# Optimization experiments

Measured on AMD Instinct MI355X. Metric: run time of the kernel, lower is better.

The kernel has to match this reference:

```python
import jax, jax.numpy as jnp
import numpy as np

SEQ_LEN = 12
E, H, BOTTLE = 64, 128, 1024
G, P = 64, 24
B = G * P
EPS = 1e-12  # F.normalize eps


def setup_inputs() -> dict:
    key = jax.random.key(0)
    ks = jax.random.split(key, 24)
    r = lambda k, s: (jax.random.normal(k, s, dtype=jnp.float32) * 0.1)
    starts = np.arange(G, dtype=np.int64) * P
    seq_start_end = jnp.asarray(np.stack([starts, starts + P], axis=1))
    return {
        'last_pos': jax.random.normal(ks[0], (B, 2), dtype=jnp.float32),
        'last_pos_rel': jax.random.normal(ks[1], (B, 2), dtype=jnp.float32),
        'h0': jax.random.normal(ks[2], (1, B, H), dtype=jnp.float32),
        'c0': jax.random.normal(ks[3], (1, B, H), dtype=jnp.float32),
        'seq_start_end': seq_start_end,
        # decoder spatial embedding Linear(2, E)
        'W_emb': r(ks[4], (E, 2)), 'b_emb': r(ks[5], (E,)),
        # LSTM(E -> H), gates ordered i,f,g,o as in torch
        'W_ih': r(ks[6], (4 * H, E)), 'W_hh': r(ks[7], (4 * H, H)),
        'b_ih': r(ks[8], (4 * H,)), 'b_hh': r(ks[9], (4 * H,)),
        # hidden2pos Linear(H, 2)
        'W_pos': r(ks[10], (2, H)), 'b_pos': r(ks[11], (2,)),
        # pool_net spatial embedding Linear(2, E)
        'Wp_emb': r(ks[12], (E, 2)), 'bp_emb': r(ks[13], (E,)),
        # pool_net mlp_pre_pool: (E+H)->512->1024, ReLU
        'Wp1': r(ks[14], (512, E + H)), 'bp1': r(ks[15], (512,)),
        'Wp2': r(ks[16], (BOTTLE, 512)), 'bp2': r(ks[17], (BOTTLE,)),
        # decoder mlp: (H+BOTTLE)->1024->H, ReLU
        'Wm1': r(ks[18], (1024, H + BOTTLE)), 'bm1': r(ks[19], (1024,)),
        'Wm2': r(ks[20], (H, 1024)), 'bm2': r(ks[21], (H,)),
    }


def reference(last_pos, last_pos_rel, h0, c0, seq_start_end,
              W_emb, b_emb, W_ih, W_hh, b_ih, b_hh, W_pos, b_pos,
              Wp_emb, bp_emb, Wp1, bp1, Wp2, bp2, Wm1, bm1, Wm2, bm2):
    batch = last_pos.shape[0]
    n_grp = seq_start_end.shape[0]
    n_ped = batch // n_grp  # equal contiguous groups -> static reshape
    h_dim = h0.shape[-1]

    def pool_net(h, pos):
        # h: [B,H], pos: [B,2]; groups are contiguous slices of size n_ped
        pos_g = pos.reshape(n_grp, n_ped, 2)
        hid_g = h.reshape(n_grp, n_ped, h_dim)
        # rel[g,i,j] = pos[g,j] - pos[g,i]  (torch repeat semantics)
        rel = pos_g[:, None, :, :] - pos_g[:, :, None, :]  # [G,P,P,2]
        nrm = jnp.linalg.norm(rel, axis=-1, keepdims=True)
        rel = rel / jnp.maximum(nrm, EPS)
        emb = rel @ Wp_emb.T + bp_emb                       # [G,P,P,E]
        hid_b = jnp.broadcast_to(hid_g[:, None, :, :], (n_grp, n_ped, n_ped, h_dim))
        x = jnp.concatenate([emb, hid_b], axis=-1)          # [G,P,P,E+H]
        x = jax.nn.relu(x @ Wp1.T + bp1)
        x = jax.nn.relu(x @ Wp2.T + bp2)                    # [G,P,P,1024]
        return jnp.max(x, axis=2).reshape(batch, -1)        # max over j

    def lstm_step(x, h, c):
        gates = x @ W_ih.T + b_ih + h @ W_hh.T + b_hh
        i, f, g, o = jnp.split(gates, 4, axis=-1)
        c = jax.nn.sigmoid(f) * c + jax.nn.sigmoid(i) * jnp.tanh(g)
        h = jax.nn.sigmoid(o) * jnp.tanh(c)
        return h, c

    def step(carry, _):
        h, c, lp, dec_in = carry
        h, c = lstm_step(dec_in, h, c)
        rel_pos = h @ W_pos.T + b_pos          # [B,2]
        curr_pos = rel_pos + lp
        pool_h = pool_net(h, curr_pos)         # [B,1024]
        dh = jnp.concatenate([h, pool_h], axis=1)
        dh = jax.nn.relu(dh @ Wm1.T + bm1)
        h = jax.nn.relu(dh @ Wm2.T + bm2)      # refreshed hidden state
        dec_in = rel_pos @ W_emb.T + b_emb
        return (h, c, curr_pos, dec_in), rel_pos

    dec_in0 = last_pos_rel @ W_emb.T + b_emb
    (h, c, lp, di), rels = jax.lax.scan(
        step, (h0[0], c0[0], last_pos, dec_in0), None, length=SEQ_LEN)
    return rels, h[None]  # ([seq_len,B,2], [1,B,H])
```

## Files before the change

### kernel.cpp

```cpp
#include <hip/hip_runtime.h>
#include <hip/hip_bf16.h>

typedef __attribute__((ext_vector_type(4))) float f32x4;
typedef __attribute__((ext_vector_type(8))) _Float16 f16x8;

static __device__ __forceinline__ unsigned short h2u(_Float16 h) {
  union { _Float16 h; unsigned short u; } v; v.h = h; return v.u;
}

#define MFMA16(a, b, c) __builtin_amdgcn_mfma_f32_16x16x32_f16(a, b, c, 0, 0, 0)


__global__ void build_wg(const float* __restrict__ W_ih, const float* __restrict__ W_hh,
                         _Float16* __restrict__ Wg) {
  int i = blockIdx.x * 256 + threadIdx.x;
  if (i < 512 * 192) {
    int r = i / 192, k = i % 192;
    float v = (k < 64) ? W_ih[r * 64 + k] : W_hh[r * 128 + (k - 64)];
    _Float16 h = (_Float16)v;
    Wg[i] = h;
    Wg[512 * 192 + i] = (_Float16)(v - (float)h);
  }
}

__global__ void build_wp1b(const float* __restrict__ Wp1, _Float16* __restrict__ W) {
  int i = blockIdx.x * 256 + threadIdx.x;
  if (i < 512 * 128) {
    int r = i >> 7, k = i & 127;
    float v = Wp1[r * 192 + 64 + k];
    _Float16 h = (_Float16)v;
    W[i] = h;
    W[512 * 128 + i] = (_Float16)(v - (float)h);
  }
}

__global__ void refrag_f32(const float* __restrict__ W, _Float16* __restrict__ F,
                           int N, int Kc) {
  int idx = blockIdx.x * 256 + threadIdx.x;
  int total = (N >> 4) * Kc * 64;
  if (idx >= total) return;
  int l = idx & 63;
  int c = (idx >> 6) % Kc;
  int T = (idx >> 6) / Kc;
  int n = T * 16 + (l & 15);
  int k = c * 32 + (l >> 4) * 8;
  int K = Kc * 32;
  const float* src = W + (size_t)n * K + k;
  _Float16* dst = F + ((size_t)((T * Kc + c) * 2) * 64 + l) * 8;
  for (int e = 0; e < 8; e++) {
    float v = src[e];
    _Float16 h = (_Float16)v;
    dst[e] = h;
    dst[512 + e] = (_Float16)(v - (float)h);
  }
}

__global__ void refrag_planes(const _Float16* __restrict__ Ws, size_t plane,
                              _Float16* __restrict__ F, int N, int Kc) {
  int idx = blockIdx.x * 256 + threadIdx.x;
  int total = (N >> 4) * Kc * 64;
  if (idx >= total) return;
  int l = idx & 63;
  int c = (idx >> 6) % Kc;
  int T = (idx >> 6) / Kc;
  int n = T * 16 + (l & 15);
  int k = c * 32 + (l >> 4) * 8;
  int K = Kc * 32;
  const _Float16* src = Ws + (size_t)n * K + k;
  _Float16* dst = F + ((size_t)((T * Kc + c) * 2) * 64 + l) * 8;
  for (int e = 0; e < 8; e++) {
    dst[e] = src[e];
    dst[512 + e] = src[plane + e];
  }
}

__global__ void build_misc(const float* __restrict__ Wp1, const float* __restrict__ Wp_emb,
                           const float* __restrict__ bp_emb, const float* __restrict__ bp1,
                           const float* __restrict__ b_ih, const float* __restrict__ b_hh,
                           float* __restrict__ Uc, float* __restrict__ c1,
                           float* __restrict__ bias_g) {
  int r = blockIdx.x * 256 + threadIdx.x;
  if (r < 512) {
    float u0 = 0.f, u1 = 0.f, cc = 0.f;
    for (int e = 0; e < 64; e++) {
      float w = Wp1[r * 192 + e];
      u0 += w * Wp_emb[e * 2 + 0];
      u1 += w * Wp_emb[e * 2 + 1];
      cc += w * bp_emb[e];
    }
    Uc[r * 2 + 0] = u0;
    Uc[r * 2 + 1] = u1;
    c1[r] = bp1[r] + cc;
    bias_g[r] = b_ih[r] + b_hh[r];
  }
}

__global__ void init_state(const float* __restrict__ lp, const float* __restrict__ lpr,
                           const float* __restrict__ h0, const float* __restrict__ c0,
                           const float* __restrict__ W_emb, const float* __restrict__ b_emb,
                           _Float16* __restrict__ A_lstm, size_t PL_AL,
                           float* __restrict__ c_state, float* __restrict__ curr_pos) {
  int row = blockIdx.x;
  int t = threadIdx.x;
  float v;
  if (t < 64) {
    v = lpr[row * 2] * W_emb[t * 2] + lpr[row * 2 + 1] * W_emb[t * 2 + 1] + b_emb[t];
  } else {
    int u = t - 64;
    v = h0[(size_t)row * 128 + u];
    c_state[(size_t)row * 128 + u] = c0[(size_t)row * 128 + u];
  }
  _Float16 h = (_Float16)v;
  A_lstm[(size_t)row * 192 + t] = h;
  A_lstm[PL_AL + (size_t)row * 192 + t] = (_Float16)(v - (float)h);
  if (t < 2) curr_pos[row * 2 + t] = lp[row * 2 + t];
}


template <int K, int RELU>
__global__ __launch_bounds__(256) void gemm_f16f(
    const _Float16* __restrict__ A, size_t aPl, int lda,
    const _Float16* __restrict__ Bf,
    const float* __restrict__ bias,
    float* __restrict__ outF, int ldoF,
    _Float16* __restrict__ outS, size_t oPl, int ldoS) {
  constexpr int Kc = K / 32;
  __shared__ _Float16 Ah[64][40], Al[64][40];
  const int tid = threadIdx.x;
  const int lane = tid & 63;
  const int wid = tid >> 6;
  const int wm = wid & 1, wn = wid >> 1;
  const int m0 = blockIdx.x * 64, n0 = blockIdx.y * 64;

  f32x4 acc[2][2];
#pragma unroll
  for (int a = 0; a < 2; a++)
#pragma unroll
    for (int b = 0; b < 2; b++) acc[a][b] = (f32x4){0.f, 0.f, 0.f, 0.f};

  const int srow = tid >> 2, sc = (tid & 3) * 8;
  const int ar = wm * 32 + (lane & 15);
  const int kk = (lane >> 4) * 8;
  const int T0 = (n0 >> 4) + wn * 2;

  for (int c = 0; c < Kc; c++) {
    const int k0 = c * 32;
    const _Float16* ap = A + (size_t)(m0 + srow) * lda + k0 + sc;
    uint4 avh = *(const uint4*)ap;
    uint4 avl = *(const uint4*)(ap + aPl);
    const _Float16* fb0 = Bf + ((size_t)((T0 * Kc + c) * 2) * 64 + lane) * 8;
    const _Float16* fb1 = Bf + ((size_t)(((T0 + 1) * Kc + c) * 2) * 64 + lane) * 8;
    f16x8 bh0 = *(const f16x8*)fb0, bl0 = *(const f16x8*)(fb0 + 512);
    f16x8 bh1 = *(const f16x8*)fb1, bl1 = *(const f16x8*)(fb1 + 512);
    *(uint4*)&Ah[srow][sc] = avh;
    *(uint4*)&Al[srow][sc] = avl;
    __syncthreads();
    f16x8 ah0 = *(const f16x8*)&Ah[ar][kk];
    f16x8 ah1 = *(const f16x8*)&Ah[ar + 16][kk];
    f16x8 al0 = *(const f16x8*)&Al[ar][kk];
    f16x8 al1 = *(const f16x8*)&Al[ar + 16][kk];
    acc[0][0] = MFMA16(ah0, bh0, acc[0][0]);
    acc[0][0] = MFMA16(ah0, bl0, acc[0][0]);
    acc[0][0] = MFMA16(al0, bh0, acc[0][0]);
    acc[0][1] = MFMA16(ah0, bh1, acc[0][1]);
    acc[0][1] = MFMA16(ah0, bl1, acc[0][1]);
    acc[0][1] = MFMA16(al0, bh1, acc[0][1]);
    acc[1][0] = MFMA16(ah1, bh0, acc[1][0]);
    acc[1][0] = MFMA16(ah1, bl0, acc[1][0]);
    acc[1][0] = MFMA16(al1, bh0, acc[1][0]);
    acc[1][1] = MFMA16(ah1, bh1, acc[1][1]);
    acc[1][1] = MFMA16(ah1, bl1, acc[1][1]);
    acc[1][1] = MFMA16(al1, bh1, acc[1][1]);
    __syncthreads();
  }
#pragma unroll
  for (int mi = 0; mi < 2; mi++)
#pragma unroll
    for (int ni = 0; ni < 2; ni++)
#pragma unroll
      for (int r = 0; r < 4; r++) {
        int row = m0 + wm * 32 + mi * 16 + (lane >> 4) * 4 + r;
        int col = n0 + wn * 32 + ni * 16 + (lane & 15);
        float v = acc[mi][ni][r];
        if (bias) v += bias[col];
        if (RELU) v = fmaxf(v, 0.f);
        if (outF) outF[(size_t)row * ldoF + col] = v;
        if (outS) {
          _Float16 h = (_Float16)v;
          outS[(size_t)row * ldoS + col] = h;
          outS[oPl + (size_t)row * ldoS + col] = (_Float16)(v - (float)h);
        }
      }
}


__global__ __launch_bounds__(256) void lstm_pointwise(
    const float* __restrict__ gates, float* __restrict__ c_state,
    _Float16* __restrict__ A_mlp, size_t PL_AM,
    float* __restrict__ curr_pos,
    float* __restrict__ rels_out,
    _Float16* __restrict__ A_lstm, size_t PL_AL,
    const float* __restrict__ W_pos, const float* __restrict__ b_pos,
    const float* __restrict__ W_emb, const float* __restrict__ b_emb) {
  __shared__ float hbuf[16][128];
  __shared__ float rp[16][2];
  int tid = threadIdx.x;
  int r = tid >> 4, l16 = tid & 15;
  int row = blockIdx.x * 16 + r;
  const float* g = gates + (size_t)row * 512;
#pragma unroll
  for (int s = 0; s < 8; s++) {
    int u = l16 + s * 16;
    float gi = g[u], gf = g[128 + u], gg = g[256 + u], go = g[384 + u];
    float si = 1.f / (1.f + expf(-gi));
    float sf = 1.f / (1.f + expf(-gf));
    float so = 1.f / (1.f + expf(-go));
    float c = sf * c_state[(size_t)row * 128 + u] + si * tanhf(gg);
    c_state[(size_t)row * 128 + u] = c;
    float h = so * tanhf(c);
    hbuf[r][u] = h;
    _Float16 hh = (_Float16)h;
    A_mlp[(size_t)row * 1152 + u] = hh;
    A_mlp[PL_AM + (size_t)row * 1152 + u] = (_Float16)(h - (float)hh);
  }
  __syncthreads();
  if (tid < 32) {
    int rr = tid >> 1, o = tid & 1;
    int rowg = blockIdx.x * 16 + rr;
    float s = b_pos[o];
    const float* w = W_pos + o * 128;
    for (int k = 0; k < 128; k++) s += hbuf[rr][k] * w[k];
    rp[rr][o] = s;
    rels_out[(size_t)rowg * 2 + o] = s;
    curr_pos[(size_t)rowg * 2 + o] += s;
  }
  __syncthreads();
#pragma unroll
  for (int s = 0; s < 4; s++) {
    int u = l16 + s * 16;
    float v = rp[r][0] * W_emb[u * 2] + rp[r][1] * W_emb[u * 2 + 1] + b_emb[u];
    _Float16 hh = (_Float16)v;
    A_lstm[(size_t)row * 192 + u] = hh;
    A_lstm[PL_AL + (size_t)row * 192 + u] = (_Float16)(v - (float)hh);
  }
}


__global__ __launch_bounds__(512) void pool_gemm(
    const float* __restrict__ hpart,
    const float* __restrict__ curr_pos,
    const float* __restrict__ Uc,
    const _Float16* __restrict__ W2f,
    const float* __restrict__ bp2,
    _Float16* __restrict__ A_mlp, size_t oPl) {
  __shared__ _Float16 Ah[96][40], Al[96][40];
  __shared__ float Us0[96], Us1[96];
  __shared__ int pool_tile[4][256];
  int b = blockIdx.x;
  int nt = b & 3;
  int it = (b >> 2) % 6;
  int g = b / 24;
  int tid = threadIdx.x;
  int lane = tid & 63, wid = tid >> 6;
  int wm = wid & 1, wn = wid >> 1;

  int* pt = &pool_tile[0][0];
  pt[tid] = 0;
  pt[tid + 512] = 0;

  if (tid < 96) {
    int r = tid;
    int i = it * 4 + r / 24;
    int j = r % 24;
    float pix = curr_pos[(g * 24 + i) * 2 + 0];
    float piy = curr_pos[(g * 24 + i) * 2 + 1];
    float dx = curr_pos[(g * 24 + j) * 2 + 0] - pix;
    float dy = curr_pos[(g * 24 + j) * 2 + 1] - piy;
    float nrm = sqrtf(dx * dx + dy * dy);
    float inv = 1.f / fmaxf(nrm, 1e-12f);
    Us0[r] = dx * inv;
    Us1[r] = dy * inv;
  }

  f32x4 acc[3][4];
#pragma unroll
  for (int a = 0; a < 3; a++)
#pragma unroll
    for (int c = 0; c < 4; c++) acc[a][c] = (f32x4){0.f, 0.f, 0.f, 0.f};

  const int kc = (2 * tid) & 31;
  const int rb = tid >> 4;

  for (int c16 = 0; c16 < 16; c16++) {
    const int k0 = c16 * 32;
    f16x8 bh[4], bl[4];
#pragma unroll
    for (int ni = 0; ni < 4; ni++) {
      int T = nt * 16 + wn * 4 + ni;
      const _Float16* fb = W2f + ((size_t)((T * 16 + c16) * 2) * 64 + lane) * 8;
      bh[ni] = *(const f16x8*)fb;
      bl[ni] = *(const f16x8*)(fb + 512);
    }
    __syncthreads();
#pragma unroll
    for (int s = 0; s < 3; s++) {
      int r = s * 32 + rb;
      int j = r % 24;
      float2 hp = *(const float2*)(hpart + ((size_t)(g * 24 + j)) * 512 + k0 + kc);
      float4 uc = *(const float4*)(Uc + (size_t)(k0 + kc) * 2);
      float u0 = Us0[r], u1 = Us1[r];
      float v0 = fmaxf(hp.x + u0 * uc.x + u1 * uc.y, 0.f);
      float v1 = fmaxf(hp.y + u0 * uc.z + u1 * uc.w, 0.f);
      _Float16 h0v = (_Float16)v0, h1v = (_Float16)v1;
      _Float16 l0v = (_Float16)(v0 - (float)h0v), l1v = (_Float16)(v1 - (float)h1v);
      *(unsigned int*)&Ah[r][kc] = (unsigned int)h2u(h0v) | ((unsigned int)h2u(h1v) << 16);
      *(unsigned int*)&Al[r][kc] = (unsigned int)h2u(l0v) | ((unsigned int)h2u(l1v) << 16);
    }
    __syncthreads();
    const int kk = (lane >> 4) * 8;
    f16x8 ah[3], al[3];
#pragma unroll
    for (int mi = 0; mi < 3; mi++) {
      int ar = wm * 48 + mi * 16 + (lane & 15);
      ah[mi] = *(const f16x8*)&Ah[ar][kk];
      al[mi] = *(const f16x8*)&Al[ar][kk];
    }
#pragma unroll
    for (int mi = 0; mi < 3; mi++)
#pragma unroll
      for (int ni = 0; ni < 4; ni++) {
        acc[mi][ni] = MFMA16(ah[mi], bh[ni], acc[mi][ni]);
        acc[mi][ni] = MFMA16(ah[mi], bl[ni], acc[mi][ni]);
        acc[mi][ni] = MFMA16(al[mi], bh[ni], acc[mi][ni]);
      }
  }
  __syncthreads();
#pragma unroll
  for (int mi = 0; mi < 3; mi++)
#pragma unroll
    for (int ni = 0; ni < 4; ni++)
#pragma unroll
      for (int r = 0; r < 4; r++) {
        int rl = wm * 48 + mi * 16 + (lane >> 4) * 4 + r;
        int il = rl / 24;
        int nl = wn * 64 + ni * 16 + (lane & 15);
        float z = fmaxf(acc[mi][ni][r] + bp2[nt * 256 + nl], 0.f);
        atomicMax(&pool_tile[il][nl], __float_as_int(z));
      }
  __syncthreads();
  for (int idx = tid; idx < 1024; idx += 512) {
    int il = idx >> 8, nl = idx & 255;
    int row = g * 24 + it * 4 + il;
    float z = __int_as_float(pool_tile[il][nl]);
    _Float16 h = (_Float16)z;
    A_mlp[(size_t)row * 1152 + 128 + nt * 256 + nl] = h;
    A_mlp[oPl + (size_t)row * 1152 + 128 + nt * 256 + nl] = (_Float16)(z - (float)h);
  }
}


extern "C" void kernel_launch(void* const* d_in, const int* in_sizes, int n_in,
                              void* d_out, int out_size, void* d_ws, size_t ws_size,
                              hipStream_t stream) {
  (void)in_sizes; (void)n_in; (void)out_size; (void)ws_size;
  const float* last_pos     = (const float*)d_in[0];
  const float* last_pos_rel = (const float*)d_in[1];
  const float* h0    = (const float*)d_in[2];
  const float* c0    = (const float*)d_in[3];
  const float* W_emb = (const float*)d_in[5];
  const float* b_emb = (const float*)d_in[6];
  const float* W_ih  = (const float*)d_in[7];
  const float* W_hh  = (const float*)d_in[8];
  const float* b_ih  = (const float*)d_in[9];
  const float* b_hh  = (const float*)d_in[10];
  const float* W_pos = (const float*)d_in[11];
  const float* b_pos = (const float*)d_in[12];
  const float* Wp_emb = (const float*)d_in[13];
  const float* bp_emb = (const float*)d_in[14];
  const float* Wp1 = (const float*)d_in[15];
  const float* bp1 = (const float*)d_in[16];
  const float* Wp2 = (const float*)d_in[17];
  const float* bp2 = (const float*)d_in[18];
  const float* Wm1 = (const float*)d_in[19];
  const float* bm1 = (const float*)d_in[20];
  const float* Wm2 = (const float*)d_in[21];
  const float* bm2 = (const float*)d_in[22];

  const size_t PL_AL = (size_t)1536 * 192;
  const size_t PL_AM = (size_t)1536 * 1152;
  const size_t PL_DH = (size_t)1536 * 1024;

  char* ws = (char*)d_ws;
  size_t off = 0;
  auto alloc = [&](size_t bytes) -> void* {
    void* p = ws + off;
    off = (off + bytes + 255) & ~(size_t)255;
    return p;
  };
  _Float16* Wg_s   = (_Float16*)alloc((size_t)512 * 192 * 2 * 2);
  _Float16* Wp1b_s = (_Float16*)alloc((size_t)512 * 128 * 2 * 2);
  _Float16* Wg_f   = (_Float16*)alloc((size_t)32 * 6 * 1024 * 2);
  _Float16* Wp1b_f = (_Float16*)alloc((size_t)32 * 4 * 1024 * 2);
  _Float16* W2f    = (_Float16*)alloc((size_t)64 * 16 * 1024 * 2);
  _Float16* Wm1_f  = (_Float16*)alloc((size_t)64 * 36 * 1024 * 2);
  _Float16* Wm2_f  = (_Float16*)alloc((size_t)8 * 32 * 1024 * 2);
  float* Uc     = (float*)alloc(512 * 2 * 4);
  float* c1     = (float*)alloc(512 * 4);
  float* bias_g = (float*)alloc(512 * 4);
  _Float16* A_lstm = (_Float16*)alloc(PL_AL * 2 * 2);
  float* gates   = (float*)alloc((size_t)1536 * 512 * 4);
  float* c_state = (float*)alloc((size_t)1536 * 128 * 4);
  _Float16* A_mlp = (_Float16*)alloc(PL_AM * 2 * 2);
  float* curr_pos = (float*)alloc(1536 * 2 * 4);
  float* hpart = (float*)alloc((size_t)1536 * 512 * 4);
  _Float16* dh = (_Float16*)alloc(PL_DH * 2 * 2);

  float* rels = (float*)d_out;
  float* h_out = ((float*)d_out) + 12 * 1536 * 2;

  build_wg<<<(98304 + 255) / 256, 256, 0, stream>>>(W_ih, W_hh, Wg_s);
  build_wp1b<<<(65536 + 255) / 256, 256, 0, stream>>>(Wp1, Wp1b_s);
  refrag_planes<<<(12288 + 255) / 256, 256, 0, stream>>>(Wg_s, 98304, Wg_f, 512, 6);
  refrag_planes<<<(8192 + 255) / 256, 256, 0, stream>>>(Wp1b_s, 65536, Wp1b_f, 512, 4);
  refrag_f32<<<(65536 + 255) / 256, 256, 0, stream>>>(Wp2, W2f, 1024, 16);
  refrag_f32<<<(147456 + 255) / 256, 256, 0, stream>>>(Wm1, Wm1_f, 1024, 36);
  refrag_f32<<<(16384 + 255) / 256, 256, 0, stream>>>(Wm2, Wm2_f, 128, 32);
  build_misc<<<2, 256, 0, stream>>>(Wp1, Wp_emb, bp_emb, bp1, b_ih, b_hh, Uc, c1, bias_g);
  init_state<<<1536, 192, 0, stream>>>(last_pos, last_pos_rel, h0, c0, W_emb, b_emb,
                                       A_lstm, PL_AL, c_state, curr_pos);

  for (int t = 0; t < 12; t++) {
    gemm_f16f<192, 0><<<dim3(24, 8), 256, 0, stream>>>(
        A_lstm, PL_AL, 192, Wg_f, bias_g, gates, 512, (_Float16*)nullptr, 0, 0);
    lstm_pointwise<<<96, 256, 0, stream>>>(gates, c_state, A_mlp, PL_AM, curr_pos,
                                           rels + (size_t)t * 1536 * 2, A_lstm, PL_AL,
                                           W_pos, b_pos, W_emb, b_emb);
    gemm_f16f<128, 0><<<dim3(24, 8), 256, 0, stream>>>(
        A_mlp, PL_AM, 1152, Wp1b_f, c1, hpart, 512, (_Float16*)nullptr, 0, 0);
    pool_gemm<<<1536, 512, 0, stream>>>(hpart, curr_pos, Uc, W2f, bp2, A_mlp, PL_AM);
    gemm_f16f<1152, 1><<<dim3(24, 16), 256, 0, stream>>>(
        A_mlp, PL_AM, 1152, Wm1_f, bm1, (float*)nullptr, 0, dh, PL_DH, 1024);
    float* houtF = (t == 11) ? h_out : (float*)nullptr;
    gemm_f16f<1024, 1><<<dim3(24, 2), 256, 0, stream>>>(
        dh, PL_DH, 1024, Wm2_f, bm2, houtF, 128, A_lstm + 64, PL_AL, 192);
  }
}
```

Measured before the change: 2.019 ms.

## Fuse LSTM pointwise into gate GEMM and fold pose projection into hpart GEMM

Interleaves the gate weight rows (i,f,g,o per hidden unit) so each GEMM tile holds all four gates of 16 units, letting the LSTM cell update run in the GEMM epilogue from shared memory. This removes the fp32 gates buffer round trip. The hidden-to-position projection and the next decoder input embedding move into the blockIdx.y==0 blocks of the hpart GEMM, which removes one launch per step. In exchange, one column of blocks does extra serial work, and the previous A_lstm embedding write is now tied to the hpart kernel.

```diff
diff --git a/kernel.cpp b/kernel.cpp
--- a/kernel.cpp
+++ b/kernel.cpp
@@ -15,8 +15,10 @@
                          _Float16* __restrict__ Wg) {
   int i = blockIdx.x * 256 + threadIdx.x;
   if (i < 512 * 192) {
-    int r = i / 192, k = i % 192;
-    float v = (k < 64) ? W_ih[r * 64 + k] : W_hh[r * 128 + (k - 64)];
+    int rp = i / 192, k = i % 192;
+    int u = rp >> 2, gate = rp & 3;
+    int sr = gate * 128 + u;
+    float v = (k < 64) ? W_ih[sr * 64 + k] : W_hh[sr * 128 + (k - 64)];
     _Float16 h = (_Float16)v;
     Wg[i] = h;
     Wg[512 * 192 + i] = (_Float16)(v - (float)h);
@@ -78,7 +80,7 @@
                            const float* __restrict__ bp_emb, const float* __restrict__ bp1,
                            const float* __restrict__ b_ih, const float* __restrict__ b_hh,
                            float* __restrict__ Uc, float* __restrict__ c1,
-                           float* __restrict__ bias_g) {
+                           float* __restrict__ bias_gi) {
   int r = blockIdx.x * 256 + threadIdx.x;
   if (r < 512) {
     float u0 = 0.f, u1 = 0.f, cc = 0.f;
@@ -91,7 +93,8 @@
     Uc[r * 2 + 0] = u0;
     Uc[r * 2 + 1] = u1;
     c1[r] = bp1[r] + cc;
-    bias_g[r] = b_ih[r] + b_hh[r];
+    int u = r >> 2, gate = r & 3;
+    bias_gi[r] = b_ih[gate * 128 + u] + b_hh[gate * 128 + u];
   }
 }
 
@@ -194,54 +197,204 @@
 }
 
 
-__global__ __launch_bounds__(256) void lstm_pointwise(
-    const float* __restrict__ gates, float* __restrict__ c_state,
-    _Float16* __restrict__ A_mlp, size_t PL_AM,
-    float* __restrict__ curr_pos,
-    float* __restrict__ rels_out,
-    _Float16* __restrict__ A_lstm, size_t PL_AL,
-    const float* __restrict__ W_pos, const float* __restrict__ b_pos,
-    const float* __restrict__ W_emb, const float* __restrict__ b_emb) {
-  __shared__ float hbuf[16][128];
-  __shared__ float rp[16][2];
-  int tid = threadIdx.x;
-  int r = tid >> 4, l16 = tid & 15;
-  int row = blockIdx.x * 16 + r;
-  const float* g = gates + (size_t)row * 512;
-#pragma unroll
-  for (int s = 0; s < 8; s++) {
-    int u = l16 + s * 16;
-    float gi = g[u], gf = g[128 + u], gg = g[256 + u], go = g[384 + u];
+__global__ __launch_bounds__(256) void gates_lstm(
+    const _Float16* __restrict__ A, size_t aPl,
+    const _Float16* __restrict__ Bf,
+    const float* __restrict__ bias,
+    float* __restrict__ c_state,
+    _Float16* __restrict__ A_mlp, size_t oPl) {
+  constexpr int Kc = 6;
+  __shared__ _Float16 Ah[64][40], Al[64][40];
+  __shared__ float sacc[64][68];
+  const int tid = threadIdx.x;
+  const int lane = tid & 63;
+  const int wid = tid >> 6;
+  const int wm = wid & 1, wn = wid >> 1;
+  const int m0 = blockIdx.x * 64, n0 = blockIdx.y * 64;
+
+  f32x4 acc[2][2];
+#pragma unroll
+  for (int a = 0; a < 2; a++)
+#pragma unroll
+    for (int b = 0; b < 2; b++) acc[a][b] = (f32x4){0.f, 0.f, 0.f, 0.f};
+
+  const int srow = tid >> 2, sc = (tid & 3) * 8;
+  const int ar = wm * 32 + (lane & 15);
+  const int kk = (lane >> 4) * 8;
+  const int T0 = (n0 >> 4) + wn * 2;
+
+  for (int c = 0; c < Kc; c++) {
+    const int k0 = c * 32;
+    const _Float16* ap = A + (size_t)(m0 + srow) * 192 + k0 + sc;
+    uint4 avh = *(const uint4*)ap;
+    uint4 avl = *(const uint4*)(ap + aPl);
+    const _Float16* fb0 = Bf + ((size_t)((T0 * Kc + c) * 2) * 64 + lane) * 8;
+    const _Float16* fb1 = Bf + ((size_t)(((T0 + 1) * Kc + c) * 2) * 64 + lane) * 8;
+    f16x8 bh0 = *(const f16x8*)fb0, bl0 = *(const f16x8*)(fb0 + 512);
+    f16x8 bh1 = *(const f16x8*)fb1, bl1 = *(const f16x8*)(fb1 + 512);
+    *(uint4*)&Ah[srow][sc] = avh;
+    *(uint4*)&Al[srow][sc] = avl;
+    __syncthreads();
+    f16x8 ah0 = *(const f16x8*)&Ah[ar][kk];
+    f16x8 ah1 = *(const f16x8*)&Ah[ar + 16][kk];
+    f16x8 al0 = *(const f16x8*)&Al[ar][kk];
+    f16x8 al1 = *(const f16x8*)&Al[ar + 16][kk];
+    acc[0][0] = MFMA16(ah0, bh0, acc[0][0]);
+    acc[0][0] = MFMA16(ah0, bl0, acc[0][0]);
+    acc[0][0] = MFMA16(al0, bh0, acc[0][0]);
+    acc[0][1] = MFMA16(ah0, bh1, acc[0][1]);
+    acc[0][1] = MFMA16(ah0, bl1, acc[0][1]);
+    acc[0][1] = MFMA16(al0, bh1, acc[0][1]);
+    acc[1][0] = MFMA16(ah1, bh0, acc[1][0]);
+    acc[1][0] = MFMA16(ah1, bl0, acc[1][0]);
+    acc[1][0] = MFMA16(al1, bh0, acc[1][0]);
+    acc[1][1] = MFMA16(ah1, bh1, acc[1][1]);
+    acc[1][1] = MFMA16(ah1, bl1, acc[1][1]);
+    acc[1][1] = MFMA16(al1, bh1, acc[1][1]);
+    __syncthreads();
+  }
+#pragma unroll
+  for (int mi = 0; mi < 2; mi++)
+#pragma unroll
+    for (int ni = 0; ni < 2; ni++)
+#pragma unroll
+      for (int r = 0; r < 4; r++) {
+        int row_l = wm * 32 + mi * 16 + (lane >> 4) * 4 + r;
+        int col_l = wn * 32 + ni * 16 + (lane & 15);
+        sacc[row_l][col_l] = acc[mi][ni][r] + bias[n0 + col_l];
+      }
+  __syncthreads();
+  const int n0u = n0 >> 2;
+#pragma unroll
+  for (int q = 0; q < 4; q++) {
+    int cell = q * 256 + tid;
+    int r_l = cell >> 4, u_l = cell & 15;
+    float gi = sacc[r_l][u_l * 4 + 0];
+    float gf = sacc[r_l][u_l * 4 + 1];
+    float gg = sacc[r_l][u_l * 4 + 2];
+    float go = sacc[r_l][u_l * 4 + 3];
+    int row = m0 + r_l, u = n0u + u_l;
     float si = 1.f / (1.f + expf(-gi));
     float sf = 1.f / (1.f + expf(-gf));
     float so = 1.f / (1.f + expf(-go));
-    float c = sf * c_state[(size_t)row * 128 + u] + si * tanhf(gg);
-    c_state[(size_t)row * 128 + u] = c;
-    float h = so * tanhf(c);
-    hbuf[r][u] = h;
+    float cst = sf * c_state[(size_t)row * 128 + u] + si * tanhf(gg);
+    c_state[(size_t)row * 128 + u] = cst;
+    float h = so * tanhf(cst);
     _Float16 hh = (_Float16)h;
     A_mlp[(size_t)row * 1152 + u] = hh;
-    A_mlp[PL_AM + (size_t)row * 1152 + u] = (_Float16)(h - (float)hh);
-  }
-  __syncthreads();
-  if (tid < 32) {
-    int rr = tid >> 1, o = tid & 1;
-    int rowg = blockIdx.x * 16 + rr;
-    float s = b_pos[o];
-    const float* w = W_pos + o * 128;
-    for (int k = 0; k < 128; k++) s += hbuf[rr][k] * w[k];
-    rp[rr][o] = s;
-    rels_out[(size_t)rowg * 2 + o] = s;
-    curr_pos[(size_t)rowg * 2 + o] += s;
-  }
-  __syncthreads();
-#pragma unroll
-  for (int s = 0; s < 4; s++) {
-    int u = l16 + s * 16;
-    float v = rp[r][0] * W_emb[u * 2] + rp[r][1] * W_emb[u * 2 + 1] + b_emb[u];
-    _Float16 hh = (_Float16)v;
-    A_lstm[(size_t)row * 192 + u] = hh;
-    A_lstm[PL_AL + (size_t)row * 192 + u] = (_Float16)(v - (float)hh);
+    A_mlp[oPl + (size_t)row * 1152 + u] = (_Float16)(h - (float)hh);
+  }
+}
+
+
+__global__ __launch_bounds__(256) void hpart_pose(
+    const _Float16* __restrict__ A, size_t aPl,
+    const _Float16* __restrict__ Bf,
+    const float* __restrict__ c1,
+    float* __restrict__ hpart,
+    const float* __restrict__ W_pos, const float* __restrict__ b_pos,
+    const float* __restrict__ W_emb, const float* __restrict__ b_emb,
+    float* __restrict__ rels_out, float* __restrict__ curr_pos,
+    _Float16* __restrict__ A_lstm, size_t alPl) {
+  constexpr int Kc = 4;
+  __shared__ _Float16 Ah[64][40], Al[64][40];
+  __shared__ float srel[64][2];
+  const int tid = threadIdx.x;
+  const int lane = tid & 63;
+  const int wid = tid >> 6;
+  const int wm = wid & 1, wn = wid >> 1;
+  const int m0 = blockIdx.x * 64, n0 = blockIdx.y * 64;
+  const int by0 = (blockIdx.y == 0);
+
+  f32x4 acc[2][2];
+#pragma unroll
+  for (int a = 0; a < 2; a++)
+#pragma unroll
+    for (int b = 0; b < 2; b++) acc[a][b] = (f32x4){0.f, 0.f, 0.f, 0.f};
+
+  const int srow = tid >> 2, sc = (tid & 3) * 8;
+  const int ar = wm * 32 + (lane & 15);
+  const int kk = (lane >> 4) * 8;
+  const int T0 = (n0 >> 4) + wn * 2;
+  float pp0 = 0.f, pp1 = 0.f;
+
+  for (int c = 0; c < Kc; c++) {
+    const int k0 = c * 32;
+    const _Float16* ap = A + (size_t)(m0 + srow) * 1152 + k0 + sc;
+    uint4 avh = *(const uint4*)ap;
+    uint4 avl = *(const uint4*)(ap + aPl);
+    if (by0) {
+      union { uint4 u; _Float16 f[8]; } uh, ul;
+      uh.u = avh; ul.u = avl;
+#pragma unroll
+      for (int e = 0; e < 8; e++) {
+        float hv = (float)uh.f[e] + (float)ul.f[e];
+        int k = k0 + sc + e;
+        pp0 += hv * W_pos[k];
+        pp1 += hv * W_pos[128 + k];
+      }
+    }
+    const _Float16* fb0 = Bf + ((size_t)((T0 * Kc + c) * 2) * 64 + lane) * 8;
+    const _Float16* fb1 = Bf + ((size_t)(((T0 + 1) * Kc + c) * 2) * 64 + lane) * 8;
+    f16x8 bh0 = *(const f16x8*)fb0, bl0 = *(const f16x8*)(fb0 + 512);
+    f16x8 bh1 = *(const f16x8*)fb1, bl1 = *(const f16x8*)(fb1 + 512);
+    *(uint4*)&Ah[srow][sc] = avh;
+    *(uint4*)&Al[srow][sc] = avl;
+    __syncthreads();
+    f16x8 ah0 = *(const f16x8*)&Ah[ar][kk];
+    f16x8 ah1 = *(const f16x8*)&Ah[ar + 16][kk];
+    f16x8 al0 = *(const f16x8*)&Al[ar][kk];
+    f16x8 al1 = *(const f16x8*)&Al[ar + 16][kk];
+    acc[0][0] = MFMA16(ah0, bh0, acc[0][0]);
+    acc[0][0] = MFMA16(ah0, bl0, acc[0][0]);
+    acc[0][0] = MFMA16(al0, bh0, acc[0][0]);
+    acc[0][1] = MFMA16(ah0, bh1, acc[0][1]);
+    acc[0][1] = MFMA16(ah0, bl1, acc[0][1]);
+    acc[0][1] = MFMA16(al0, bh1, acc[0][1]);
+    acc[1][0] = MFMA16(ah1, bh0, acc[1][0]);
+    acc[1][0] = MFMA16(ah1, bl0, acc[1][0]);
+    acc[1][0] = MFMA16(al1, bh0, acc[1][0]);
+    acc[1][1] = MFMA16(ah1, bh1, acc[1][1]);
+    acc[1][1] = MFMA16(ah1, bl1, acc[1][1]);
+    acc[1][1] = MFMA16(al1, bh1, acc[1][1]);
+    __syncthreads();
+  }
+#pragma unroll
+  for (int mi = 0; mi < 2; mi++)
+#pragma unroll
+    for (int ni = 0; ni < 2; ni++)
+#pragma unroll
+      for (int r = 0; r < 4; r++) {
+        int row = m0 + wm * 32 + mi * 16 + (lane >> 4) * 4 + r;
+        int col = n0 + wn * 32 + ni * 16 + (lane & 15);
+        hpart[(size_t)row * 512 + col] = acc[mi][ni][r] + c1[col];
+      }
+  if (by0) {
+    pp0 += __shfl_xor(pp0, 1);
+    pp0 += __shfl_xor(pp0, 2);
+    pp1 += __shfl_xor(pp1, 1);
+    pp1 += __shfl_xor(pp1, 2);
+    if ((tid & 3) == 0) {
+      int row = m0 + srow;
+      float r0 = pp0 + b_pos[0], r1 = pp1 + b_pos[1];
+      rels_out[(size_t)row * 2 + 0] = r0;
+      rels_out[(size_t)row * 2 + 1] = r1;
+      curr_pos[(size_t)row * 2 + 0] += r0;
+      curr_pos[(size_t)row * 2 + 1] += r1;
+      srel[srow][0] = r0;
+      srel[srow][1] = r1;
+    }
+    __syncthreads();
+#pragma unroll
+    for (int q = 0; q < 16; q++) {
+      int idx = q * 256 + tid;
+      int r_l = idx >> 6, cc = idx & 63;
+      int row = m0 + r_l;
+      float v = srel[r_l][0] * W_emb[cc * 2] + srel[r_l][1] * W_emb[cc * 2 + 1] + b_emb[cc];
+      _Float16 hh = (_Float16)v;
+      A_lstm[(size_t)row * 192 + cc] = hh;
+      A_lstm[alPl + (size_t)row * 192 + cc] = (_Float16)(v - (float)hh);
+    }
   }
 }
 
@@ -397,18 +550,17 @@
     off = (off + bytes + 255) & ~(size_t)255;
     return p;
   };
-  _Float16* Wg_s   = (_Float16*)alloc((size_t)512 * 192 * 2 * 2);
+  _Float16* Wgi_s  = (_Float16*)alloc((size_t)512 * 192 * 2 * 2);
   _Float16* Wp1b_s = (_Float16*)alloc((size_t)512 * 128 * 2 * 2);
-  _Float16* Wg_f   = (_Float16*)alloc((size_t)32 * 6 * 1024 * 2);
+  _Float16* Wgi_f  = (_Float16*)alloc((size_t)32 * 6 * 1024 * 2);
   _Float16* Wp1b_f = (_Float16*)alloc((size_t)32 * 4 * 1024 * 2);
   _Float16* W2f    = (_Float16*)alloc((size_t)64 * 16 * 1024 * 2);
   _Float16* Wm1_f  = (_Float16*)alloc((size_t)64 * 36 * 1024 * 2);
   _Float16* Wm2_f  = (_Float16*)alloc((size_t)8 * 32 * 1024 * 2);
-  float* Uc     = (float*)alloc(512 * 2 * 4);
-  float* c1     = (float*)alloc(512 * 4);
-  float* bias_g = (float*)alloc(512 * 4);
+  float* Uc      = (float*)alloc(512 * 2 * 4);
+  float* c1      = (float*)alloc(512 * 4);
+  float* bias_gi = (float*)alloc(512 * 4);
   _Float16* A_lstm = (_Float16*)alloc(PL_AL * 2 * 2);
-  float* gates   = (float*)alloc((size_t)1536 * 512 * 4);
   float* c_state = (float*)alloc((size_t)1536 * 128 * 4);
   _Float16* A_mlp = (_Float16*)alloc(PL_AM * 2 * 2);
   float* curr_pos = (float*)alloc(1536 * 2 * 4);
@@ -418,25 +570,24 @@
   float* rels = (float*)d_out;
   float* h_out = ((float*)d_out) + 12 * 1536 * 2;
 
-  build_wg<<<(98304 + 255) / 256, 256, 0, stream>>>(W_ih, W_hh, Wg_s);
+  build_wg<<<(98304 + 255) / 256, 256, 0, stream>>>(W_ih, W_hh, Wgi_s);
   build_wp1b<<<(65536 + 255) / 256, 256, 0, stream>>>(Wp1, Wp1b_s);
-  refrag_planes<<<(12288 + 255) / 256, 256, 0, stream>>>(Wg_s, 98304, Wg_f, 512, 6);
+  refrag_planes<<<(12288 + 255) / 256, 256, 0, stream>>>(Wgi_s, 98304, Wgi_f, 512, 6);
   refrag_planes<<<(8192 + 255) / 256, 256, 0, stream>>>(Wp1b_s, 65536, Wp1b_f, 512, 4);
   refrag_f32<<<(65536 + 255) / 256, 256, 0, stream>>>(Wp2, W2f, 1024, 16);
   refrag_f32<<<(147456 + 255) / 256, 256, 0, stream>>>(Wm1, Wm1_f, 1024, 36);
   refrag_f32<<<(16384 + 255) / 256, 256, 0, stream>>>(Wm2, Wm2_f, 128, 32);
-  build_misc<<<2, 256, 0, stream>>>(Wp1, Wp_emb, bp_emb, bp1, b_ih, b_hh, Uc, c1, bias_g);
+  build_misc<<<2, 256, 0, stream>>>(Wp1, Wp_emb, bp_emb, bp1, b_ih, b_hh, Uc, c1, bias_gi);
   init_state<<<1536, 192, 0, stream>>>(last_pos, last_pos_rel, h0, c0, W_emb, b_emb,
                                        A_lstm, PL_AL, c_state, curr_pos);
 
   for (int t = 0; t < 12; t++) {
-    gemm_f16f<192, 0><<<dim3(24, 8), 256, 0, stream>>>(
-        A_lstm, PL_AL, 192, Wg_f, bias_g, gates, 512, (_Float16*)nullptr, 0, 0);
-    lstm_pointwise<<<96, 256, 0, stream>>>(gates, c_state, A_mlp, PL_AM, curr_pos,
-                                           rels + (size_t)t * 1536 * 2, A_lstm, PL_AL,
-                                           W_pos, b_pos, W_emb, b_emb);
-    gemm_f16f<128, 0><<<dim3(24, 8), 256, 0, stream>>>(
-        A_mlp, PL_AM, 1152, Wp1b_f, c1, hpart, 512, (_Float16*)nullptr, 0, 0);
+    gates_lstm<<<dim3(24, 8), 256, 0, stream>>>(A_lstm, PL_AL, Wgi_f, bias_gi,
+                                                c_state, A_mlp, PL_AM);
+    hpart_pose<<<dim3(24, 8), 256, 0, stream>>>(A_mlp, PL_AM, Wp1b_f, c1, hpart,
+                                                W_pos, b_pos, W_emb, b_emb,
+                                                rels + (size_t)t * 1536 * 2, curr_pos,
+                                                A_lstm, PL_AL);
     pool_gemm<<<1536, 512, 0, stream>>>(hpart, curr_pos, Uc, W2f, bp2, A_mlp, PL_AM);
     gemm_f16f<1152, 1><<<dim3(24, 16), 256, 0, stream>>>(
         A_mlp, PL_AM, 1152, Wm1_f, bm1, (float*)nullptr, 0, dh, PL_DH, 1024);
```

Result: faster. 1.924 ms (-4.7%).
